# Kernel optimization log

Measured on AMD Instinct MI355X. Metric: run time of the kernel, lower is better.

Reference implementation:

```python
import jax, jax.numpy as jnp
import numpy as np

D = 1024
KERNEL = 4

def setup_inputs() -> dict:
    key = jax.random.key(0)
    ks = jax.random.split(key, 8)
    B, L, d = 4, 8192, D
    x = jax.random.normal(ks[0], (B, L, d), dtype=jnp.float32)
    conv_weight = jax.random.normal(ks[1], (d, 1, KERNEL), dtype=jnp.float32) * 0.02
    conv_bias = jnp.zeros((d,), dtype=jnp.float32)
    lim = 1.0 / np.sqrt(d)
    Wr_w = jax.random.uniform(ks[2], (d, d), jnp.float32, -lim, lim)
    Wr_b = jax.random.uniform(ks[3], (d,), jnp.float32, -lim, lim)
    Wi_w = jax.random.uniform(ks[4], (d, d), jnp.float32, -lim, lim)
    Wi_b = jax.random.uniform(ks[5], (d,), jnp.float32, -lim, lim)
    log_a = jnp.full((d,), 7.5, dtype=jnp.float32)
    out_w = jax.random.uniform(ks[6], (d, d), jnp.float32, -lim, lim)
    norm_w = jnp.ones((d,), dtype=jnp.float32)
    return {"x": x, "conv_weight": conv_weight, "conv_bias": conv_bias,
            "Wr_w": Wr_w, "Wr_b": Wr_b, "Wi_w": Wi_w, "Wi_b": Wi_b,
            "log_a": log_a, "out_w": out_w, "norm_w": norm_w}

def _causal_depthwise_conv(x, w, b):
    # x: [B,L,d], w: [d,1,K], b: [d]. out[t] = sum_k w[:,0,k] * x[t-3+k] + b
    B, L, d = x.shape
    xp = jnp.pad(x, ((0, 0), (KERNEL - 1, 0), (0, 0)))
    out = b[None, None, :]
    for k in range(KERNEL):  # small fixed kernel loop
        out = out + xp[:, k:k + L, :] * w[:, 0, k][None, None, :]
    return out

def _parallel_scan(a_t, b_t):
    # h_t = a_t * h_{t-1} + b_t via log-space cumsum; float32 throughout
    a = a_t.astype(jnp.float32)
    b = b_t.astype(jnp.float32)
    log_A = jnp.clip(jnp.cumsum(jnp.log(jnp.clip(a, 1e-7)), axis=1), -80.0, None)
    A = jnp.exp(log_A)
    h = A * jnp.cumsum(b * jnp.exp(-log_A), axis=1)
    return h.astype(a_t.dtype)

def _rmsnorm(x, w, eps=1e-6):
    ms = jnp.mean(jnp.square(x.astype(jnp.float32)), axis=-1, keepdims=True)
    return (x * jax.lax.rsqrt(ms + eps)).astype(x.dtype) * w

def reference(x, conv_weight, conv_bias, Wr_w, Wr_b, Wi_w, Wi_b, log_a, out_w, norm_w):
    x_conv = _causal_depthwise_conv(x, conv_weight, conv_bias)          # [B,L,d]
    r_t = jax.nn.sigmoid(x_conv @ Wr_w.T + Wr_b)
    i_t = jax.nn.sigmoid(x_conv @ Wi_w.T + Wi_b)
    a_base = jax.nn.sigmoid(log_a.astype(jnp.float32)).astype(x.dtype)
    a_t = jnp.power(a_base[None, None, :], 8.0 * r_t)
    b_t = jnp.sqrt(jnp.clip(1.0 - a_t * a_t, 1e-6, None)) * (i_t * x_conv)
    h = _parallel_scan(a_t, b_t)
    return _rmsnorm(h @ out_w.T, norm_w)
```

## Files before the change

kernel.cpp:

```cpp
#include <hip/hip_runtime.h>
#include <hip/hip_bf16.h>

#define D 1024
#define KW 4
#define SEQL 8192
#define BATCH 4
#define MROWS (BATCH*SEQL)
#define SEG 32
#define NSEG (SEQL/SEG)
#define NCHAIN (BATCH*D)

using bf16 = __hip_bfloat16;
typedef __attribute__((ext_vector_type(8))) short bf16x8_t;
typedef __attribute__((ext_vector_type(4))) float f32x4_t;

__device__ __forceinline__ float sigmoid_f(float x){ return 1.0f/(1.0f + __expf(-x)); }

__device__ __forceinline__ void gload_lds16(const bf16* g, bf16* l){
  __builtin_amdgcn_global_load_lds(
    (const __attribute__((address_space(1))) unsigned int*)g,
    (__attribute__((address_space(3))) unsigned int*)l,
    16, 0, 0);
}

__device__ __forceinline__ void bf16x2_unpack(unsigned int u, float& lo, float& hi){
  union { unsigned int i; float f; } a, b;
  a.i = (u & 0xffffu) << 16;
  b.i = u & 0xffff0000u;
  lo = a.f; hi = b.f;
}
__device__ __forceinline__ unsigned int bf16x2_pack(float lo, float hi){
  unsigned short l = __builtin_bit_cast(unsigned short, __float2bfloat16(lo));
  unsigned short h = __builtin_bit_cast(unsigned short, __float2bfloat16(hi));
  return (unsigned int)l | ((unsigned int)h << 16);
}

__global__ __launch_bounds__(256) void prep_k(const float* __restrict__ Wr, const float* __restrict__ Wi,
                                              const float* __restrict__ Wrb, const float* __restrict__ Wib,
                                              const float* __restrict__ Wo, const float* __restrict__ log_a,
                                              bf16* __restrict__ W1, bf16* __restrict__ Wob,
                                              float* __restrict__ b1, float* __restrict__ c1buf){
  int idx = blockIdx.x*256 + threadIdx.x;
  if (idx < 2*D*D){
    int n   = idx >> 10;
    int col = idx & 1023;
    int c   = n >> 1;
    float v = (n & 1) ? Wi[(size_t)c*D + col] : Wr[(size_t)c*D + col];
    W1[idx] = __float2bfloat16(v);
  } else if (idx < 3*D*D){
    int j = idx - 2*D*D;
    Wob[j] = __float2bfloat16(Wo[j]);
  }
  if (idx < 2*D){
    int c = idx >> 1;
    b1[idx] = (idx & 1) ? Wib[c] : Wrb[c];
  }
  if (idx < D){
    c1buf[idx] = -8.f * log1pf(__expf(-log_a[idx]));
  }
}

__global__ __launch_bounds__(256) void conv_k(const float* __restrict__ x, const float* __restrict__ w,
                                              const float* __restrict__ bias,
                                              unsigned int* __restrict__ xcb){
  int idx = blockIdx.x*256 + threadIdx.x;
  int c4 = idx & 255;
  int c  = c4 * 4;
  int mm = idx >> 8;
  int m  = mm * 2;
  int l  = m & (SEQL-1);
  const float* wp = w + c*KW;
  f32x4_t t0 = *(const f32x4_t*)(wp);
  f32x4_t t1 = *(const f32x4_t*)(wp + 4);
  f32x4_t t2 = *(const f32x4_t*)(wp + 8);
  f32x4_t t3 = *(const f32x4_t*)(wp + 12);
  f32x4_t bb = *(const f32x4_t*)(bias + c);
  const float* xm = x + (size_t)m*D + c;
  f32x4_t z  = (f32x4_t){0.f,0.f,0.f,0.f};
  f32x4_t r4 = *(const f32x4_t*)(xm + D);
  f32x4_t r3 = *(const f32x4_t*)(xm);
  f32x4_t r2 = (l>=1)? *(const f32x4_t*)(xm - D)   : z;
  f32x4_t r1 = (l>=2)? *(const f32x4_t*)(xm - 2*D) : z;
  f32x4_t r0 = (l>=3)? *(const f32x4_t*)(xm - 3*D) : z;
  float a0 = bb[0] + t0[0]*r0[0] + t0[1]*r1[0] + t0[2]*r2[0] + t0[3]*r3[0];
  float a1 = bb[1] + t1[0]*r0[1] + t1[1]*r1[1] + t1[2]*r2[1] + t1[3]*r3[1];
  float a2 = bb[2] + t2[0]*r0[2] + t2[1]*r1[2] + t2[2]*r2[2] + t2[3]*r3[2];
  float a3 = bb[3] + t3[0]*r0[3] + t3[1]*r1[3] + t3[2]*r2[3] + t3[3]*r3[3];
  float b0 = bb[0] + t0[0]*r1[0] + t0[1]*r2[0] + t0[2]*r3[0] + t0[3]*r4[0];
  float b1v= bb[1] + t1[0]*r1[1] + t1[1]*r2[1] + t1[2]*r3[1] + t1[3]*r4[1];
  float b2 = bb[2] + t2[0]*r1[2] + t2[1]*r2[2] + t2[2]*r3[2] + t2[3]*r4[2];
  float b3 = bb[3] + t3[0]*r1[3] + t3[1]*r2[3] + t3[2]*r3[3] + t3[3]*r4[3];
  uint2 o0, o1;
  o0.x = bf16x2_pack(a0, a1); o0.y = bf16x2_pack(a2, a3);
  o1.x = bf16x2_pack(b0, b1v); o1.y = bf16x2_pack(b2, b3);
  *(uint2*)(xcb + (size_t)m*512 + 2*c4)       = o0;
  *(uint2*)(xcb + (size_t)(m+1)*512 + 2*c4)   = o1;
}

template<typename OutT> __device__ __forceinline__ void store_cvt(OutT* p, float v);
template<> __device__ __forceinline__ void store_cvt<float>(float* p, float v){ *p = v; }
template<> __device__ __forceinline__ void store_cvt<bf16>(bf16* p, float v){ *p = __float2bfloat16(v); }

#define MFMA_BF16(a,b,c) __builtin_amdgcn_mfma_f32_16x16x32_bf16((a),(b),(c),0,0,0)

#define GPHASE(buf, q, STAGE_STMT, WAIT_STMT) do{                         \
    bf16x8_t a0 = rdA(buf, 2*(q),   0);                                   \
    bf16x8_t a1 = rdA(buf, 2*(q),   1);                                   \
    bf16x8_t a2 = rdA(buf, 2*(q)+1, 0);                                   \
    bf16x8_t a3 = rdA(buf, 2*(q)+1, 1);                                   \
    if ((q) == 0){                                                        \
      b00 = rdB(buf,0,0); b01 = rdB(buf,0,1);                             \
      b10 = rdB(buf,1,0); b11 = rdB(buf,1,1);                             \
      b20 = rdB(buf,2,0); b21 = rdB(buf,2,1);                             \
      b30 = rdB(buf,3,0); b31 = rdB(buf,3,1);                             \
    }                                                                     \
    STAGE_STMT;                                                           \
    WAIT_STMT;                                                            \
    __builtin_amdgcn_s_barrier();                                         \
    asm volatile("s_waitcnt lgkmcnt(0)" ::: "memory");                    \
    __builtin_amdgcn_s_setprio(1);                                        \
    acc[2*(q)  ][0] = MFMA_BF16(a0, b00, acc[2*(q)  ][0]);                \
    acc[2*(q)  ][1] = MFMA_BF16(a0, b10, acc[2*(q)  ][1]);                \
    acc[2*(q)  ][2] = MFMA_BF16(a0, b20, acc[2*(q)  ][2]);                \
    acc[2*(q)  ][3] = MFMA_BF16(a0, b30, acc[2*(q)  ][3]);                \
    acc[2*(q)+1][0] = MFMA_BF16(a2, b00, acc[2*(q)+1][0]);                \
    acc[2*(q)+1][1] = MFMA_BF16(a2, b10, acc[2*(q)+1][1]);                \
    acc[2*(q)+1][2] = MFMA_BF16(a2, b20, acc[2*(q)+1][2]);                \
    acc[2*(q)+1][3] = MFMA_BF16(a2, b30, acc[2*(q)+1][3]);                \
    acc[2*(q)  ][0] = MFMA_BF16(a1, b01, acc[2*(q)  ][0]);                \
    acc[2*(q)  ][1] = MFMA_BF16(a1, b11, acc[2*(q)  ][1]);                \
    acc[2*(q)  ][2] = MFMA_BF16(a1, b21, acc[2*(q)  ][2]);                \
    acc[2*(q)  ][3] = MFMA_BF16(a1, b31, acc[2*(q)  ][3]);                \
    acc[2*(q)+1][0] = MFMA_BF16(a3, b01, acc[2*(q)+1][0]);                \
    acc[2*(q)+1][1] = MFMA_BF16(a3, b11, acc[2*(q)+1][1]);                \
    acc[2*(q)+1][2] = MFMA_BF16(a3, b21, acc[2*(q)+1][2]);                \
    acc[2*(q)+1][3] = MFMA_BF16(a3, b31, acc[2*(q)+1][3]);                \
    __builtin_amdgcn_s_setprio(0);                                        \
    __builtin_amdgcn_s_barrier();                                         \
}while(0)

#define WAIT_STEADY do{ if (it + 1 < nIter) asm volatile("s_waitcnt vmcnt(4)" ::: "memory"); \
                        else                asm volatile("s_waitcnt vmcnt(0)" ::: "memory"); }while(0)

template<typename OutT, bool HB, bool FUSE>
__global__ __launch_bounds__(512, 2) void gemm256(const bf16* __restrict__ A, const bf16* __restrict__ B,
                                                  const float* __restrict__ bias, OutT* __restrict__ C,
                                                  int M, int N, int K,
                                                  const bf16* __restrict__ xv_src,
                                                  const float* __restrict__ c1buf){
  __shared__ alignas(128) bf16 Asm[2][256*64];
  __shared__ alignas(128) bf16 Bsm[2][256*64];
  const int t    = threadIdx.x;
  const int wave = t >> 6, lane = t & 63;
  const int wm   = wave >> 2, wn = wave & 3;
  const int lrow = lane & 15, quad = lane >> 4;

  const int nbn = N >> 8;
  const int cpx = gridDim.x >> 3;
  const int bid = blockIdx.x;
  const int swz = (bid & 7) * cpx + (bid >> 3);
  const int m0  = (swz / nbn) << 8;
  const int n0  = (swz % nbn) << 8;

  const int srow = wave*8 + (lane >> 3);
  const int scol = (((lane & 7) ^ (srow & 7)) << 3);

  auto stageA = [&](int tile, int half, int buf){
    const bf16* g = A + (size_t)(m0 + half*128 + srow)*K + tile*64 + scol;
    bf16* l = &Asm[buf][half*128*64 + wave*8*64];
    gload_lds16(g, l);
    gload_lds16(g + (size_t)64*K, l + 64*64);
  };
  auto stageB = [&](int tile, int half, int buf){
    const bf16* g = B + (size_t)(n0 + half*128 + srow)*K + tile*64 + scol;
    bf16* l = &Bsm[buf][half*128*64 + wave*8*64];
    gload_lds16(g, l);
    gload_lds16(g + (size_t)64*K, l + 64*64);
  };
  auto rdA = [&](int buf, int fi, int ks)->bf16x8_t{
    return *(const bf16x8_t*)&Asm[buf][(wm*128 + fi*16 + lrow)*64 + ((((ks)*4 + quad) ^ (lrow & 7)) << 3)];
  };
  auto rdB = [&](int buf, int j, int ks)->bf16x8_t{
    return *(const bf16x8_t*)&Bsm[buf][(wn*64 + j*16 + lrow)*64 + ((((ks)*4 + quad) ^ (lrow & 7)) << 3)];
  };

  f32x4_t acc[8][4];
  #pragma unroll
  for (int i=0;i<8;i++)
    #pragma unroll
    for (int j=0;j<4;j++) acc[i][j] = (f32x4_t){0.f,0.f,0.f,0.f};
  bf16x8_t b00,b01,b10,b11,b20,b21,b30,b31;

  const int nt    = K >> 6;
  const int nIter = nt >> 1;

  stageB(0, 0, 0); stageB(0, 1, 0);
  stageA(0, 0, 0); stageA(0, 1, 0);
  stageB(1, 0, 1); stageB(1, 1, 1);
  asm volatile("s_waitcnt vmcnt(4)" ::: "memory");
  __builtin_amdgcn_s_barrier();

  for (int it = 0; it < nIter; ++it){
    const int t1 = 2*it + 1, t2 = 2*it + 2, t3 = 2*it + 3;
    const bool ok2 = (t2 < nt), ok3 = (t3 < nt);
    GPHASE(0, 0, stageA(t1, 0, 1), );
    GPHASE(0, 1, stageA(t1, 1, 1), );
    GPHASE(0, 2, if (ok2) stageB(t2, 0, 0), );
    GPHASE(0, 3, if (ok2) stageB(t2, 1, 0), WAIT_STEADY);
    GPHASE(1, 0, if (ok2) stageA(t2, 0, 0), );
    GPHASE(1, 1, if (ok2) stageA(t2, 1, 0), );
    GPHASE(1, 2, if (ok3) stageB(t3, 0, 1), );
    GPHASE(1, 3, if (ok3) stageB(t3, 1, 1), WAIT_STEADY);
  }

  constexpr int ROWP = 256 + 16/(int)sizeof(OutT);
  OutT* tile = (OutT*)&Asm[0][0];
  const int trow = t >> 4;
  const int tcol = (t & 15) * 16;
  float bvj[4];
  #pragma unroll
  for (int j=0;j<4;j++) bvj[j] = HB ? bias[n0 + wn*64 + j*16 + lrow] : 0.f;
  const int grow = m0 + (trow >> 4)*128 + (trow & 15);

  int cbase = 0;
  float c1v[8];
  if constexpr (FUSE){
    cbase = (n0 + tcol) >> 1;
    f32x4_t c1a = *(const f32x4_t*)(c1buf + cbase);
    f32x4_t c1b = *(const f32x4_t*)(c1buf + cbase + 4);
    #pragma unroll
    for (int k=0;k<4;k++){ c1v[k] = c1a[k]; c1v[4+k] = c1b[k]; }
  }

  #pragma unroll
  for (int i=0;i<8;i++){
    __builtin_amdgcn_s_barrier();
    #pragma unroll
    for (int j=0;j<4;j++){
      int lcol = wn*64 + j*16 + lrow;
      #pragma unroll
      for (int r=0;r<4;r++)
        store_cvt(&tile[(wm*16 + quad*4 + r)*ROWP + lcol], acc[i][j][r] + bvj[j]);
    }
    __builtin_amdgcn_s_barrier();
    const int4* lp = (const int4*)&tile[trow*ROWP + tcol];
    if constexpr (FUSE){
      int4 w0 = lp[0], w1 = lp[1];
      unsigned int lw[8] = {(unsigned)w0.x,(unsigned)w0.y,(unsigned)w0.z,(unsigned)w0.w,
                            (unsigned)w1.x,(unsigned)w1.y,(unsigned)w1.z,(unsigned)w1.w};
      const int row = grow + i*16;
      uint4 xv4 = *(const uint4*)(xv_src + (size_t)row*D + cbase);
      float xv[8];
      bf16x2_unpack(xv4.x, xv[0], xv[1]); bf16x2_unpack(xv4.y, xv[2], xv[3]);
      bf16x2_unpack(xv4.z, xv[4], xv[5]); bf16x2_unpack(xv4.w, xv[6], xv[7]);
      unsigned int out[8];
      #pragma unroll
      for (int k=0;k<8;k++){
        float zr, zi;
        bf16x2_unpack(lw[k], zr, zi);
        float a  = __expf(c1v[k] * sigmoid_f(zr));
        float bt = sqrtf(fmaxf(1.f - a*a, 1e-6f)) * sigmoid_f(zi) * xv[k];
        out[k] = bf16x2_pack(1.f - a, bt);
      }
      int4* gp = (int4*)&C[(size_t)row*N + n0 + tcol];
      gp[0] = make_int4(out[0],out[1],out[2],out[3]);
      gp[1] = make_int4(out[4],out[5],out[6],out[7]);
    } else {
      int4* gp = (int4*)&C[(size_t)(grow + i*16)*N + n0 + tcol];
      #pragma unroll
      for (int q=0; q<(int)sizeof(OutT); ++q) gp[q] = lp[q];
    }
  }
}

__global__ __launch_bounds__(256) void scan1_k(const unsigned int* __restrict__ ab,
                                               float* __restrict__ AprodT, float* __restrict__ HendT){
  int idx = blockIdx.x*256 + threadIdx.x;
  int c4 = idx & 255;
  int c  = c4*4;
  int bs = idx >> 8;
  int s  = bs & (NSEG-1);
  int b  = bs >> 8;
  size_t m0 = (size_t)b*SEQL + (size_t)s*SEG;
  float A[4] = {1.f,1.f,1.f,1.f};
  float h[4] = {0.f,0.f,0.f,0.f};
  #pragma unroll 4
  for (int l=0; l<SEG; l++){
    uint4 u = *(const uint4*)(ab + (m0 + l)*1024 + 4*c4);
    unsigned int uu[4] = {u.x, u.y, u.z, u.w};
    #pragma unroll
    for (int j=0;j<4;j++){
      float dv, bt;
      bf16x2_unpack(uu[j], dv, bt);
      float a = 1.f - dv;
      A[j] *= a;
      h[j]  = fmaf(a, h[j], bt);
    }
  }
  size_t tbase = (size_t)s*NCHAIN + (size_t)b*D + c;
  *(f32x4_t*)(AprodT + tbase) = (f32x4_t){A[0],A[1],A[2],A[3]};
  *(f32x4_t*)(HendT  + tbase) = (f32x4_t){h[0],h[1],h[2],h[3]};
}

__global__ __launch_bounds__(256) void scan2_k(const float* __restrict__ AprodT, const float* __restrict__ HendT,
                                               float* __restrict__ carryT){
  int gid   = blockIdx.x*256 + threadIdx.x;
  int chain = gid >> 6;
  int lane  = gid & 63;
  int s0    = lane*4;
  float a[4], e[4];
  #pragma unroll
  for (int k=0;k<4;k++){
    a[k] = AprodT[(size_t)(s0+k)*NCHAIN + chain];
    e[k] = HendT [(size_t)(s0+k)*NCHAIN + chain];
  }
  float A = a[0], H = e[0];
  #pragma unroll
  for (int k=1;k<4;k++){ H = fmaf(a[k], H, e[k]); A *= a[k]; }
  #pragma unroll
  for (int off=1; off<64; off<<=1){
    float Ao = __shfl_up(A, off, 64);
    float Ho = __shfl_up(H, off, 64);
    if (lane >= off){ H = fmaf(A, Ho, H); A = A*Ao; }
  }
  float Hx = __shfl_up(H, 1, 64);
  if (lane == 0) Hx = 0.f;
  float h = Hx;
  #pragma unroll
  for (int k=0;k<4;k++){
    carryT[(size_t)(s0+k)*NCHAIN + chain] = h;
    h = fmaf(a[k], h, e[k]);
  }
}

__global__ __launch_bounds__(256) void scan3_k(const unsigned int* __restrict__ ab,
                                               unsigned int* __restrict__ hout,
                                               const float* __restrict__ carryT){
  int idx = blockIdx.x*256 + threadIdx.x;
  int c4 = idx & 255;
  int c  = c4*4;
  int bs = idx >> 8;
  int s  = bs & (NSEG-1);
  int b  = bs >> 8;
  size_t m0 = (size_t)b*SEQL + (size_t)s*SEG;
  f32x4_t h4 = *(const f32x4_t*)(carryT + (size_t)s*NCHAIN + (size_t)b*D + c);
  float h[4] = {h4[0], h4[1], h4[2], h4[3]};
  #pragma unroll 4
  for (int l=0; l<SEG; l++){
    size_t m = m0 + l;
    uint4 u = *(const uint4*)(ab + m*1024 + 4*c4);
    unsigned int uu[4] = {u.x, u.y, u.z, u.w};
    #pragma unroll
    for (int j=0;j<4;j++){
      float dv, bt;
      bf16x2_unpack(uu[j], dv, bt);
      h[j] = fmaf(1.f - dv, h[j], bt);
    }
    uint2 o;
    o.x = bf16x2_pack(h[0], h[1]);
    o.y = bf16x2_pack(h[2], h[3]);
    *(uint2*)(hout + m*512 + 2*c4) = o;
  }
}

__global__ __launch_bounds__(256) void rms_k(float* __restrict__ y, const float* __restrict__ nw){
  int wave = threadIdx.x >> 6, lane = threadIdx.x & 63;
  size_t row = (size_t)blockIdx.x*4 + wave;
  float* yr = y + row*D;
  f32x4_t v[4];
  #pragma unroll
  for (int q=0;q<4;q++) v[q] = *(const f32x4_t*)(yr + q*256 + lane*4);
  float ss = 0.f;
  #pragma unroll
  for (int q=0;q<4;q++) ss += v[q][0]*v[q][0] + v[q][1]*v[q][1] + v[q][2]*v[q][2] + v[q][3]*v[q][3];
  #pragma unroll
  for (int off=32; off>0; off>>=1) ss += __shfl_xor(ss, off, 64);
  float scale = rsqrtf(ss * (1.f/D) + 1e-6f);
  #pragma unroll
  for (int q=0;q<4;q++){
    f32x4_t w = *(const f32x4_t*)(nw + q*256 + lane*4);
    f32x4_t o;
    #pragma unroll
    for (int k=0;k<4;k++) o[k] = v[q][k]*scale*w[k];
    *(f32x4_t*)(yr + q*256 + lane*4) = o;
  }
}

extern "C" void kernel_launch(void* const* d_in, const int* in_sizes, int n_in,
                              void* d_out, int out_size, void* d_ws, size_t ws_size,
                              hipStream_t stream) {
  const float* x     = (const float*)d_in[0];
  const float* convw = (const float*)d_in[1];
  const float* convb = (const float*)d_in[2];
  const float* Wr_w  = (const float*)d_in[3];
  const float* Wr_b  = (const float*)d_in[4];
  const float* Wi_w  = (const float*)d_in[5];
  const float* Wi_b  = (const float*)d_in[6];
  const float* log_a = (const float*)d_in[7];
  const float* out_w = (const float*)d_in[8];
  const float* norm_w= (const float*)d_in[9];

  char* ws = (char*)d_ws;
  size_t off = 0;
  auto alloc = [&](size_t bytes)->char*{ char* p = ws + off; off += (bytes + 255) & ~(size_t)255; return p; };

  bf16*  xcb   = (bf16*) alloc((size_t)MROWS*D*2);
  bf16*  ab    = (bf16*) alloc((size_t)MROWS*2*D*2);
  bf16*  W1    = (bf16*) alloc((size_t)2*D*D*2);
  bf16*  Wob   = (bf16*) alloc((size_t)D*D*2);
  float* b1    = (float*)alloc((size_t)2*D*4);
  float* c1buf = (float*)alloc((size_t)D*4);
  float* AprodT= (float*)alloc((size_t)NSEG*NCHAIN*4);
  float* HendT = (float*)alloc((size_t)NSEG*NCHAIN*4);
  float* carryT= (float*)alloc((size_t)NSEG*NCHAIN*4);
  float* y     = (float*)d_out;

  prep_k<<<dim3((3*D*D + 255)/256), dim3(256), 0, stream>>>(Wr_w, Wi_w, Wr_b, Wi_b, out_w, log_a, W1, Wob, b1, c1buf);
  conv_k<<<dim3((MROWS/2)*(D/4)/256), dim3(256), 0, stream>>>(x, convw, convb, (unsigned int*)xcb);
  gemm256<bf16, true, true><<<dim3((MROWS/256)*((2*D)/256)), dim3(512), 0, stream>>>(xcb, W1, b1, ab, MROWS, 2*D, D, xcb, c1buf);
  scan1_k<<<dim3(BATCH*NSEG*(D/4)/256), dim3(256), 0, stream>>>((const unsigned int*)ab, AprodT, HendT);
  scan2_k<<<dim3(NCHAIN*64/256), dim3(256), 0, stream>>>(AprodT, HendT, carryT);
  scan3_k<<<dim3(BATCH*NSEG*(D/4)/256), dim3(256), 0, stream>>>((const unsigned int*)ab, (unsigned int*)xcb, carryT);
  gemm256<float, false, false><<<dim3((MROWS/256)*(D/256)), dim3(512), 0, stream>>>(xcb, Wob, nullptr, y, MROWS, D, D, nullptr, nullptr);
  rms_k<<<dim3(MROWS/4), dim3(256), 0, stream>>>(y, norm_w);
}
```

Baseline: 657.8 us.

## Fuse three scan phases into one cooperative kernel and merge prep with conv

Result: slower. 912.5 us (+38.7%).

```diff
diff --git a/kernel.cpp b/kernel.cpp
--- a/kernel.cpp
+++ b/kernel.cpp
@@ -1,5 +1,8 @@
 #include <hip/hip_runtime.h>
 #include <hip/hip_bf16.h>
+#include <hip/hip_cooperative_groups.h>
+
+namespace cg = cooperative_groups;
 
 #define D 1024
 #define KW 4
@@ -9,6 +12,8 @@
 #define SEG 32
 #define NSEG (SEQL/SEG)
 #define NCHAIN (BATCH*D)
+#define CONVBLKS ((MROWS/2)*(D/4)/256)
+#define PREPBLKS ((3*D*D + 255)/256)
 
 using bf16 = __hip_bfloat16;
 typedef __attribute__((ext_vector_type(8))) short bf16x8_t;
@@ -35,66 +40,68 @@
   return (unsigned int)l | ((unsigned int)h << 16);
 }
 
-__global__ __launch_bounds__(256) void prep_k(const float* __restrict__ Wr, const float* __restrict__ Wi,
-                                              const float* __restrict__ Wrb, const float* __restrict__ Wib,
-                                              const float* __restrict__ Wo, const float* __restrict__ log_a,
-                                              bf16* __restrict__ W1, bf16* __restrict__ Wob,
-                                              float* __restrict__ b1, float* __restrict__ c1buf){
-  int idx = blockIdx.x*256 + threadIdx.x;
-  if (idx < 2*D*D){
-    int n   = idx >> 10;
-    int col = idx & 1023;
-    int c   = n >> 1;
-    float v = (n & 1) ? Wi[(size_t)c*D + col] : Wr[(size_t)c*D + col];
-    W1[idx] = __float2bfloat16(v);
-  } else if (idx < 3*D*D){
-    int j = idx - 2*D*D;
-    Wob[j] = __float2bfloat16(Wo[j]);
-  }
-  if (idx < 2*D){
-    int c = idx >> 1;
-    b1[idx] = (idx & 1) ? Wib[c] : Wrb[c];
-  }
-  if (idx < D){
-    c1buf[idx] = -8.f * log1pf(__expf(-log_a[idx]));
-  }
-}
-
-__global__ __launch_bounds__(256) void conv_k(const float* __restrict__ x, const float* __restrict__ w,
-                                              const float* __restrict__ bias,
-                                              unsigned int* __restrict__ xcb){
-  int idx = blockIdx.x*256 + threadIdx.x;
-  int c4 = idx & 255;
-  int c  = c4 * 4;
-  int mm = idx >> 8;
-  int m  = mm * 2;
-  int l  = m & (SEQL-1);
-  const float* wp = w + c*KW;
-  f32x4_t t0 = *(const f32x4_t*)(wp);
-  f32x4_t t1 = *(const f32x4_t*)(wp + 4);
-  f32x4_t t2 = *(const f32x4_t*)(wp + 8);
-  f32x4_t t3 = *(const f32x4_t*)(wp + 12);
-  f32x4_t bb = *(const f32x4_t*)(bias + c);
-  const float* xm = x + (size_t)m*D + c;
-  f32x4_t z  = (f32x4_t){0.f,0.f,0.f,0.f};
-  f32x4_t r4 = *(const f32x4_t*)(xm + D);
-  f32x4_t r3 = *(const f32x4_t*)(xm);
-  f32x4_t r2 = (l>=1)? *(const f32x4_t*)(xm - D)   : z;
-  f32x4_t r1 = (l>=2)? *(const f32x4_t*)(xm - 2*D) : z;
-  f32x4_t r0 = (l>=3)? *(const f32x4_t*)(xm - 3*D) : z;
-  float a0 = bb[0] + t0[0]*r0[0] + t0[1]*r1[0] + t0[2]*r2[0] + t0[3]*r3[0];
-  float a1 = bb[1] + t1[0]*r0[1] + t1[1]*r1[1] + t1[2]*r2[1] + t1[3]*r3[1];
-  float a2 = bb[2] + t2[0]*r0[2] + t2[1]*r1[2] + t2[2]*r2[2] + t2[3]*r3[2];
-  float a3 = bb[3] + t3[0]*r0[3] + t3[1]*r1[3] + t3[2]*r2[3] + t3[3]*r3[3];
-  float b0 = bb[0] + t0[0]*r1[0] + t0[1]*r2[0] + t0[2]*r3[0] + t0[3]*r4[0];
-  float b1v= bb[1] + t1[0]*r1[1] + t1[1]*r2[1] + t1[2]*r3[1] + t1[3]*r4[1];
-  float b2 = bb[2] + t2[0]*r1[2] + t2[1]*r2[2] + t2[2]*r3[2] + t2[3]*r4[2];
-  float b3 = bb[3] + t3[0]*r1[3] + t3[1]*r2[3] + t3[2]*r3[3] + t3[3]*r4[3];
-  uint2 o0, o1;
-  o0.x = bf16x2_pack(a0, a1); o0.y = bf16x2_pack(a2, a3);
-  o1.x = bf16x2_pack(b0, b1v); o1.y = bf16x2_pack(b2, b3);
-  *(uint2*)(xcb + (size_t)m*512 + 2*c4)       = o0;
-  *(uint2*)(xcb + (size_t)(m+1)*512 + 2*c4)   = o1;
+__global__ __launch_bounds__(256) void convprep_k(const float* __restrict__ x, const float* __restrict__ w,
+                                                  const float* __restrict__ bias,
+                                                  unsigned int* __restrict__ xcb,
+                                                  const float* __restrict__ Wr, const float* __restrict__ Wi,
+                                                  const float* __restrict__ Wrb, const float* __restrict__ Wib,
+                                                  const float* __restrict__ Wo, const float* __restrict__ log_a,
+                                                  bf16* __restrict__ W1, bf16* __restrict__ Wob,
+                                                  float* __restrict__ b1, float* __restrict__ c1buf){
+  int bid = blockIdx.x;
+  if (bid < CONVBLKS){
+    int idx = bid*256 + threadIdx.x;
+    int c4 = idx & 255;
+    int c  = c4 * 4;
+    int mm = idx >> 8;
+    int m  = mm * 2;
+    int l  = m & (SEQL-1);
+    const float* wp = w + c*KW;
+    f32x4_t t0 = *(const f32x4_t*)(wp);
+    f32x4_t t1 = *(const f32x4_t*)(wp + 4);
+    f32x4_t t2 = *(const f32x4_t*)(wp + 8);
+    f32x4_t t3 = *(const f32x4_t*)(wp + 12);
+    f32x4_t bb = *(const f32x4_t*)(bias + c);
+    const float* xm = x + (size_t)m*D + c;
+    f32x4_t z  = (f32x4_t){0.f,0.f,0.f,0.f};
+    f32x4_t r4 = *(const f32x4_t*)(xm + D);
+    f32x4_t r3 = *(const f32x4_t*)(xm);
+    f32x4_t r2 = (l>=1)? *(const f32x4_t*)(xm - D)   : z;
+    f32x4_t r1 = (l>=2)? *(const f32x4_t*)(xm - 2*D) : z;
+    f32x4_t r0 = (l>=3)? *(const f32x4_t*)(xm - 3*D) : z;
+    float a0 = bb[0] + t0[0]*r0[0] + t0[1]*r1[0] + t0[2]*r2[0] + t0[3]*r3[0];
+    float a1 = bb[1] + t1[0]*r0[1] + t1[1]*r1[1] + t1[2]*r2[1] + t1[3]*r3[1];
+    float a2 = bb[2] + t2[0]*r0[2] + t2[1]*r1[2] + t2[2]*r2[2] + t2[3]*r3[2];
+    float a3 = bb[3] + t3[0]*r0[3] + t3[1]*r1[3] + t3[2]*r2[3] + t3[3]*r3[3];
+    float b0 = bb[0] + t0[0]*r1[0] + t0[1]*r2[0] + t0[2]*r3[0] + t0[3]*r4[0];
+    float b1v= bb[1] + t1[0]*r1[1] + t1[1]*r2[1] + t1[2]*r3[1] + t1[3]*r4[1];
+    float b2 = bb[2] + t2[0]*r1[2] + t2[1]*r2[2] + t2[2]*r3[2] + t2[3]*r4[2];
+    float b3 = bb[3] + t3[0]*r1[3] + t3[1]*r2[3] + t3[2]*r3[3] + t3[3]*r4[3];
+    uint2 o0, o1;
+    o0.x = bf16x2_pack(a0, a1); o0.y = bf16x2_pack(a2, a3);
+    o1.x = bf16x2_pack(b0, b1v); o1.y = bf16x2_pack(b2, b3);
+    *(uint2*)(xcb + (size_t)m*512 + 2*c4)       = o0;
+    *(uint2*)(xcb + (size_t)(m+1)*512 + 2*c4)   = o1;
+  } else {
+    int idx = (bid - CONVBLKS)*256 + threadIdx.x;
+    if (idx < 2*D*D){
+      int n   = idx >> 10;
+      int col = idx & 1023;
+      int c   = n >> 1;
+      float v = (n & 1) ? Wi[(size_t)c*D + col] : Wr[(size_t)c*D + col];
+      W1[idx] = __float2bfloat16(v);
+    } else if (idx < 3*D*D){
+      int j = idx - 2*D*D;
+      Wob[j] = __float2bfloat16(Wo[j]);
+    }
+    if (idx < 2*D){
+      int c = idx >> 1;
+      b1[idx] = (idx & 1) ? Wib[c] : Wrb[c];
+    }
+    if (idx < D){
+      c1buf[idx] = -8.f * log1pf(__expf(-log_a[idx]));
+    }
+  }
 }
 
 template<typename OutT> __device__ __forceinline__ void store_cvt(OutT* p, float v);
@@ -258,9 +265,12 @@
       for (int k=0;k<8;k++){
         float zr, zi;
         bf16x2_unpack(lw[k], zr, zi);
-        float a  = __expf(c1v[k] * sigmoid_f(zr));
-        float bt = sqrtf(fmaxf(1.f - a*a, 1e-6f)) * sigmoid_f(zi) * xv[k];
-        out[k] = bf16x2_pack(1.f - a, bt);
+        float tt = c1v[k] * sigmoid_f(zr);
+        float dd = -tt * fmaf(0.5f, tt, 1.0f);
+        if (tt < -0.03f) dd = 1.f - __expf(tt);
+        float omaa = dd * (2.f - dd);
+        float bt = sqrtf(fmaxf(omaa, 1e-6f)) * sigmoid_f(zi) * xv[k];
+        out[k] = bf16x2_pack(dd, bt);
       }
       int4* gp = (int4*)&C[(size_t)row*N + n0 + tcol];
       gp[0] = make_int4(out[0],out[1],out[2],out[3]);
@@ -273,8 +283,11 @@
   }
 }
 
-__global__ __launch_bounds__(256) void scan1_k(const unsigned int* __restrict__ ab,
-                                               float* __restrict__ AprodT, float* __restrict__ HendT){
+__global__ __launch_bounds__(256, 4) void scanF_k(const unsigned int* __restrict__ ab,
+                                                  unsigned int* __restrict__ hout,
+                                                  float* __restrict__ AprodT, float* __restrict__ HendT,
+                                                  float* __restrict__ carryT){
+  cg::grid_group grid = cg::this_grid();
   int idx = blockIdx.x*256 + threadIdx.x;
   int c4 = idx & 255;
   int c  = c4*4;
@@ -282,84 +295,78 @@
   int s  = bs & (NSEG-1);
   int b  = bs >> 8;
   size_t m0 = (size_t)b*SEQL + (size_t)s*SEG;
-  float A[4] = {1.f,1.f,1.f,1.f};
-  float h[4] = {0.f,0.f,0.f,0.f};
-  #pragma unroll 4
-  for (int l=0; l<SEG; l++){
-    uint4 u = *(const uint4*)(ab + (m0 + l)*1024 + 4*c4);
-    unsigned int uu[4] = {u.x, u.y, u.z, u.w};
-    #pragma unroll
-    for (int j=0;j<4;j++){
-      float dv, bt;
-      bf16x2_unpack(uu[j], dv, bt);
-      float a = 1.f - dv;
-      A[j] *= a;
-      h[j]  = fmaf(a, h[j], bt);
-    }
-  }
   size_t tbase = (size_t)s*NCHAIN + (size_t)b*D + c;
-  *(f32x4_t*)(AprodT + tbase) = (f32x4_t){A[0],A[1],A[2],A[3]};
-  *(f32x4_t*)(HendT  + tbase) = (f32x4_t){h[0],h[1],h[2],h[3]};
-}
-
-__global__ __launch_bounds__(256) void scan2_k(const float* __restrict__ AprodT, const float* __restrict__ HendT,
-                                               float* __restrict__ carryT){
-  int gid   = blockIdx.x*256 + threadIdx.x;
-  int chain = gid >> 6;
-  int lane  = gid & 63;
-  int s0    = lane*4;
-  float a[4], e[4];
-  #pragma unroll
-  for (int k=0;k<4;k++){
-    a[k] = AprodT[(size_t)(s0+k)*NCHAIN + chain];
-    e[k] = HendT [(size_t)(s0+k)*NCHAIN + chain];
-  }
-  float A = a[0], H = e[0];
-  #pragma unroll
-  for (int k=1;k<4;k++){ H = fmaf(a[k], H, e[k]); A *= a[k]; }
-  #pragma unroll
-  for (int off=1; off<64; off<<=1){
-    float Ao = __shfl_up(A, off, 64);
-    float Ho = __shfl_up(H, off, 64);
-    if (lane >= off){ H = fmaf(A, Ho, H); A = A*Ao; }
-  }
-  float Hx = __shfl_up(H, 1, 64);
-  if (lane == 0) Hx = 0.f;
-  float h = Hx;
-  #pragma unroll
-  for (int k=0;k<4;k++){
-    carryT[(size_t)(s0+k)*NCHAIN + chain] = h;
-    h = fmaf(a[k], h, e[k]);
-  }
-}
-
-__global__ __launch_bounds__(256) void scan3_k(const unsigned int* __restrict__ ab,
-                                               unsigned int* __restrict__ hout,
-                                               const float* __restrict__ carryT){
-  int idx = blockIdx.x*256 + threadIdx.x;
-  int c4 = idx & 255;
-  int c  = c4*4;
-  int bs = idx >> 8;
-  int s  = bs & (NSEG-1);
-  int b  = bs >> 8;
-  size_t m0 = (size_t)b*SEQL + (size_t)s*SEG;
-  f32x4_t h4 = *(const f32x4_t*)(carryT + (size_t)s*NCHAIN + (size_t)b*D + c);
-  float h[4] = {h4[0], h4[1], h4[2], h4[3]};
-  #pragma unroll 4
-  for (int l=0; l<SEG; l++){
-    size_t m = m0 + l;
-    uint4 u = *(const uint4*)(ab + m*1024 + 4*c4);
-    unsigned int uu[4] = {u.x, u.y, u.z, u.w};
-    #pragma unroll
-    for (int j=0;j<4;j++){
-      float dv, bt;
-      bf16x2_unpack(uu[j], dv, bt);
-      h[j] = fmaf(1.f - dv, h[j], bt);
-    }
-    uint2 o;
-    o.x = bf16x2_pack(h[0], h[1]);
-    o.y = bf16x2_pack(h[2], h[3]);
-    *(uint2*)(hout + m*512 + 2*c4) = o;
+
+  {
+    float A[4] = {1.f,1.f,1.f,1.f};
+    float h[4] = {0.f,0.f,0.f,0.f};
+    #pragma unroll 4
+    for (int l=0; l<SEG; l++){
+      uint4 u = *(const uint4*)(ab + (m0 + l)*1024 + 4*c4);
+      unsigned int uu[4] = {u.x, u.y, u.z, u.w};
+      #pragma unroll
+      for (int j=0;j<4;j++){
+        float dv, bt;
+        bf16x2_unpack(uu[j], dv, bt);
+        float a = 1.f - dv;
+        A[j] *= a;
+        h[j]  = fmaf(a, h[j], bt);
+      }
+    }
+    *(f32x4_t*)(AprodT + tbase) = (f32x4_t){A[0],A[1],A[2],A[3]};
+    *(f32x4_t*)(HendT  + tbase) = (f32x4_t){h[0],h[1],h[2],h[3]};
+  }
+  grid.sync();
+
+  {
+    int chain = idx >> 6;
+    int lane  = idx & 63;
+    int s0    = lane*4;
+    float a[4], e[4];
+    #pragma unroll
+    for (int k=0;k<4;k++){
+      a[k] = AprodT[(size_t)(s0+k)*NCHAIN + chain];
+      e[k] = HendT [(size_t)(s0+k)*NCHAIN + chain];
+    }
+    float A = a[0], H = e[0];
+    #pragma unroll
+    for (int k=1;k<4;k++){ H = fmaf(a[k], H, e[k]); A *= a[k]; }
+    #pragma unroll
+    for (int off=1; off<64; off<<=1){
+      float Ao = __shfl_up(A, off, 64);
+      float Ho = __shfl_up(H, off, 64);
+      if (lane >= off){ H = fmaf(A, Ho, H); A = A*Ao; }
+    }
+    float Hx = __shfl_up(H, 1, 64);
+    if (lane == 0) Hx = 0.f;
+    float h = Hx;
+    #pragma unroll
+    for (int k=0;k<4;k++){
+      carryT[(size_t)(s0+k)*NCHAIN + chain] = h;
+      h = fmaf(a[k], h, e[k]);
+    }
+  }
+  grid.sync();
+
+  {
+    f32x4_t h4 = *(const f32x4_t*)(carryT + tbase);
+    float h[4] = {h4[0], h4[1], h4[2], h4[3]};
+    #pragma unroll 4
+    for (int l=0; l<SEG; l++){
+      size_t m = m0 + l;
+      uint4 u = *(const uint4*)(ab + m*1024 + 4*c4);
+      unsigned int uu[4] = {u.x, u.y, u.z, u.w};
+      #pragma unroll
+      for (int j=0;j<4;j++){
+        float dv, bt;
+        bf16x2_unpack(uu[j], dv, bt);
+        h[j] = fmaf(1.f - dv, h[j], bt);
+      }
+      uint2 o;
+      o.x = bf16x2_pack(h[0], h[1]);
+      o.y = bf16x2_pack(h[2], h[3]);
+      *(uint2*)(hout + m*512 + 2*c4) = o;
+    }
   }
 }
 
@@ -415,12 +422,16 @@
   float* carryT= (float*)alloc((size_t)NSEG*NCHAIN*4);
   float* y     = (float*)d_out;
 
-  prep_k<<<dim3((3*D*D + 255)/256), dim3(256), 0, stream>>>(Wr_w, Wi_w, Wr_b, Wi_b, out_w, log_a, W1, Wob, b1, c1buf);
-  conv_k<<<dim3((MROWS/2)*(D/4)/256), dim3(256), 0, stream>>>(x, convw, convb, (unsigned int*)xcb);
+  convprep_k<<<dim3(CONVBLKS + PREPBLKS), dim3(256), 0, stream>>>(
+      x, convw, convb, (unsigned int*)xcb,
+      Wr_w, Wi_w, Wr_b, Wi_b, out_w, log_a, W1, Wob, b1, c1buf);
   gemm256<bf16, true, true><<<dim3((MROWS/256)*((2*D)/256)), dim3(512), 0, stream>>>(xcb, W1, b1, ab, MROWS, 2*D, D, xcb, c1buf);
-  scan1_k<<<dim3(BATCH*NSEG*(D/4)/256), dim3(256), 0, stream>>>((const unsigned int*)ab, AprodT, HendT);
-  scan2_k<<<dim3(NCHAIN*64/256), dim3(256), 0, stream>>>(AprodT, HendT, carryT);
-  scan3_k<<<dim3(BATCH*NSEG*(D/4)/256), dim3(256), 0, stream>>>((const unsigned int*)ab, (unsigned int*)xcb, carryT);
+  {
+    const unsigned int* ab_c = (const unsigned int*)ab;
+    unsigned int* hout_c = (unsigned int*)xcb;
+    void* kargs[] = {(void*)&ab_c, (void*)&hout_c, (void*)&AprodT, (void*)&HendT, (void*)&carryT};
+    hipLaunchCooperativeKernel((const void*)scanF_k, dim3(BATCH*NSEG*(D/4)/256), dim3(256), kargs, 0, stream);
+  }
   gemm256<float, false, false><<<dim3((MROWS/256)*(D/256)), dim3(512), 0, stream>>>(xcb, Wob, nullptr, y, MROWS, D, D, nullptr, nullptr);
   rms_k<<<dim3(MROWS/4), dim3(256), 0, stream>>>(y, norm_w);
 }
```
